# Optimization experiments

Measured on AMD Instinct MI355X. Metric: run time of the kernel, lower is better.

The kernel has to match this reference:

```python
import jax, jax.numpy as jnp
import numpy as np

NEG_INF = -1e9  # masked_fill value from the torch module


def setup_inputs() -> dict:
    key = jax.random.key(0)
    ks = jax.random.split(key, 6)
    n_edges, hidden = 100000, 256
    n_paths, max_len = 20000, 16
    edge_emb = jax.random.normal(ks[0], (n_edges, hidden), dtype=jnp.float32)
    paths = jax.random.randint(ks[1], (n_paths, max_len), 0, n_edges)
    path_lens = jax.random.randint(ks[2], (n_paths,), 0, max_len)  # +1 in reference -> 1..max_len
    path_mask = jax.random.randint(ks[3], (n_paths,), 0, 2)
    # nn.Linear(hidden, 1) parameters
    W = jax.random.normal(ks[4], (1, hidden), dtype=jnp.float32) / np.sqrt(hidden)
    b = jax.random.normal(ks[5], (1,), dtype=jnp.float32) * 0.01
    return {"edge_emb": edge_emb, "paths": paths, "path_lens": path_lens,
            "path_mask": path_mask, "W": W, "b": b, "deterministic": 1}


def reference(edge_emb, paths, path_lens, path_mask, W, b, deterministic):
    # ragged per-path mean: emulate `for p in paths: edge_emb[p].mean(0)` with padded gather
    lens = path_lens + 1                                   # [P], 1..max_len
    pos = jnp.arange(paths.shape[1])                        # [L]
    valid = pos[None, :] < lens[:, None]                    # [P, L]
    gathered = edge_emb[paths]                              # [P, L, H]
    z = jnp.sum(jnp.where(valid[..., None], gathered, 0.0), axis=1) / lens[:, None].astype(edge_emb.dtype)  # [P, H]
    logits = z @ W[0] + b[0]                                # [P]  (Linear(H,1).squeeze())
    logits = jnp.where(path_mask == 0, NEG_INF, logits)
    logp = jax.nn.log_softmax(logits)
    if deterministic:
        p = jnp.argmax(logits)
    else:
        p = jax.random.categorical(jax.random.key(42), logits)
    logprob = logp[p]
    return (p, logprob, z[p])
```

## Files before the change

kernel.cpp:

```cpp
#include <hip/hip_runtime.h>
#include <math.h>
#include <limits.h>

#define NEG_INF -1e9f

__global__ __launch_bounds__(256) void k_edge_dot(
    const float* __restrict__ emb, const float* __restrict__ W,
    float* __restrict__ s, int* __restrict__ counter, int n_edges)
{
    if (blockIdx.x == 0 && threadIdx.x == 0) *counter = 0;
    int wave = (blockIdx.x * (int)blockDim.x + (int)threadIdx.x) >> 6;
    int lane = threadIdx.x & 63;
    if (wave >= n_edges) return;
    const float4 e = ((const float4*)emb)[wave * 64 + lane];
    const float4 w = ((const float4*)W)[lane];
    float d = e.x * w.x + e.y * w.y + e.z * w.z + e.w * w.w;
#pragma unroll
    for (int off = 32; off; off >>= 1) d += __shfl_down(d, off, 64);
    if (lane == 0) s[wave] = d;
}

__global__ __launch_bounds__(256) void k_fused(
    const float* __restrict__ s, const int* __restrict__ paths,
    const int* __restrict__ path_lens, const int* __restrict__ path_mask,
    const float* __restrict__ b, const float* __restrict__ emb,
    float* __restrict__ pmax, int* __restrict__ pidx, float* __restrict__ psum,
    int* __restrict__ counter, float* __restrict__ out,
    int n_paths, int max_len)
{
    __shared__ float rv[4];
    __shared__ int   ri[4];
    __shared__ float rs[4];
    __shared__ float s_bm, s_M, s_S;
    __shared__ int   s_bi, s_P, s_last;

    const int tid = threadIdx.x, lane = tid & 63, wv = tid >> 6;
    const int p = blockIdx.x * 256 + tid;

    float v = -INFINITY; int vi = INT_MAX;
    if (p < n_paths) {
        vi = p;
        if (path_mask[p] == 0) {
            v = NEG_INF;
        } else {
            int len = path_lens[p] + 1;
            float acc = 0.f;
            if (max_len == 16) {
                const int4* pp4 = (const int4*)(paths + (size_t)p * 16);
                int4 a0 = pp4[0], a1 = pp4[1], a2 = pp4[2], a3 = pp4[3];
                int idx[16] = { a0.x, a0.y, a0.z, a0.w, a1.x, a1.y, a1.z, a1.w,
                                a2.x, a2.y, a2.z, a2.w, a3.x, a3.y, a3.z, a3.w };
#pragma unroll
                for (int j = 0; j < 16; ++j) {
                    float t = s[idx[j]];
                    acc += (j < len) ? t : 0.f;
                }
            } else {
                const int* pp = paths + (size_t)p * max_len;
                for (int j = 0; j < len; ++j) acc += s[pp[j]];
            }
            v = acc / (float)len + b[0];
        }
    }

    float bv = v; int bi = vi;
#pragma unroll
    for (int off = 32; off; off >>= 1) {
        float ov = __shfl_down(bv, off, 64);
        int   oi = __shfl_down(bi, off, 64);
        if (ov > bv || (ov == bv && oi < bi)) { bv = ov; bi = oi; }
    }
    if (lane == 0) { rv[wv] = bv; ri[wv] = bi; }
    __syncthreads();
    if (tid == 0) {
        float mv = rv[0]; int mi = ri[0];
        for (int w = 1; w < 4; ++w)
            if (rv[w] > mv || (rv[w] == mv && ri[w] < mi)) { mv = rv[w]; mi = ri[w]; }
        s_bm = mv; s_bi = mi;
    }
    __syncthreads();
    const float bm = s_bm;

    float se = expf(v - bm);
#pragma unroll
    for (int off = 32; off; off >>= 1) se += __shfl_down(se, off, 64);
    if (lane == 0) rs[wv] = se;
    __syncthreads();

    if (tid == 0) {
        pmax[blockIdx.x] = bm;
        pidx[blockIdx.x] = s_bi;
        psum[blockIdx.x] = rs[0] + rs[1] + rs[2] + rs[3];
        __threadfence();
        int tk = atomicAdd(counter, 1);
        s_last = (tk == (int)gridDim.x - 1) ? 1 : 0;
    }
    __syncthreads();
    if (!s_last) return;
    __threadfence();

    const int nb = gridDim.x;
    float mv = -INFINITY; int mi = INT_MAX;
    for (int i = tid; i < nb; i += 256) {
        float t = pmax[i]; int ti = pidx[i];
        if (t > mv || (t == mv && ti < mi)) { mv = t; mi = ti; }
    }
#pragma unroll
    for (int off = 32; off; off >>= 1) {
        float ov = __shfl_down(mv, off, 64);
        int   oi = __shfl_down(mi, off, 64);
        if (ov > mv || (ov == mv && oi < mi)) { mv = ov; mi = oi; }
    }
    if (lane == 0) { rv[wv] = mv; ri[wv] = mi; }
    __syncthreads();
    if (tid == 0) {
        float M = rv[0]; int P = ri[0];
        for (int w = 1; w < 4; ++w)
            if (rv[w] > M || (rv[w] == M && ri[w] < P)) { M = rv[w]; P = ri[w]; }
        s_M = M; s_P = P;
    }
    __syncthreads();
    const float M = s_M; const int P = s_P;

    float sp = 0.f;
    for (int i = tid; i < nb; i += 256)
        sp += psum[i] * expf(pmax[i] - M);
#pragma unroll
    for (int off = 32; off; off >>= 1) sp += __shfl_down(sp, off, 64);
    if (lane == 0) rs[wv] = sp;
    __syncthreads();
    if (tid == 0) s_S = rs[0] + rs[1] + rs[2] + rs[3];
    __syncthreads();

    const int lenP = path_lens[P] + 1;
    const int* pp = paths + (size_t)P * max_len;
    float acc = 0.f;
    for (int j = 0; j < lenP; ++j)
        acc += emb[(size_t)pp[j] * 256 + tid];
    out[2 + tid] = acc / (float)lenP;
    if (tid == 0) { out[0] = (float)P; out[1] = -logf(s_S); }
}

extern "C" void kernel_launch(void* const* d_in, const int* in_sizes, int n_in,
                              void* d_out, int out_size, void* d_ws, size_t ws_size,
                              hipStream_t stream) {
    const float* emb       = (const float*)d_in[0];
    const int*   paths     = (const int*)  d_in[1];
    const int*   path_lens = (const int*)  d_in[2];
    const int*   path_mask = (const int*)  d_in[3];
    const float* W         = (const float*)d_in[4];
    const float* b         = (const float*)d_in[5];

    int hidden  = in_sizes[4];
    int n_edges = in_sizes[0] / hidden;
    int n_paths = in_sizes[2];
    int max_len = in_sizes[1] / n_paths;

    int blocks2 = (n_paths + 255) / 256;

    float* s       = (float*)d_ws;
    float* pmax    = s + n_edges;
    float* psum    = pmax + blocks2;
    int*   pidx    = (int*)(psum + blocks2);
    int*   counter = pidx + blocks2;

    int blocks1 = (n_edges * 64 + 255) / 256;
    k_edge_dot<<<blocks1, 256, 0, stream>>>(emb, W, s, counter, n_edges);

    k_fused<<<blocks2, 256, 0, stream>>>(s, paths, path_lens, path_mask, b, emb,
                                         pmax, pidx, psum, counter,
                                         (float*)d_out, n_paths, max_len);
}
```

Before: 166.0 us.

## Fuse edge dot into path kernel with one wave per path gathering full rows

Removes the separate per-edge dot-product pass over the whole embedding table. Each wave now handles one path: it gathers the full embedding rows with float4 loads, averages them, and dots the mean with W in registers. The grid grows from about 80 blocks of 256 paths to thousands of 4-path blocks, which should hide the latency of the random gathers, and a tiny init kernel resets the counter. In exchange, every valid path reads whole 1KB rows instead of single scalars, and the final block must reduce many more partial results.

```diff
diff --git a/kernel.cpp b/kernel.cpp
--- a/kernel.cpp
+++ b/kernel.cpp
@@ -4,47 +4,31 @@
 
 #define NEG_INF -1e9f
 
-__global__ __launch_bounds__(256) void k_edge_dot(
-    const float* __restrict__ emb, const float* __restrict__ W,
-    float* __restrict__ s, int* __restrict__ counter, int n_edges)
-{
-    if (blockIdx.x == 0 && threadIdx.x == 0) *counter = 0;
-    int wave = (blockIdx.x * (int)blockDim.x + (int)threadIdx.x) >> 6;
-    int lane = threadIdx.x & 63;
-    if (wave >= n_edges) return;
-    const float4 e = ((const float4*)emb)[wave * 64 + lane];
-    const float4 w = ((const float4*)W)[lane];
-    float d = e.x * w.x + e.y * w.y + e.z * w.z + e.w * w.w;
-#pragma unroll
-    for (int off = 32; off; off >>= 1) d += __shfl_down(d, off, 64);
-    if (lane == 0) s[wave] = d;
-}
+__global__ void k_init(int* __restrict__ counter) { *counter = 0; }
 
-__global__ __launch_bounds__(256) void k_fused(
-    const float* __restrict__ s, const int* __restrict__ paths,
+__global__ __launch_bounds__(256) void k_all(
+    const float* __restrict__ emb, const int* __restrict__ paths,
     const int* __restrict__ path_lens, const int* __restrict__ path_mask,
-    const float* __restrict__ b, const float* __restrict__ emb,
+    const float* __restrict__ W, const float* __restrict__ b,
     float* __restrict__ pmax, int* __restrict__ pidx, float* __restrict__ psum,
     int* __restrict__ counter, float* __restrict__ out,
     int n_paths, int max_len)
 {
-    __shared__ float rv[4];
-    __shared__ int   ri[4];
-    __shared__ float rs[4];
-    __shared__ float s_bm, s_M, s_S;
-    __shared__ int   s_bi, s_P, s_last;
+    __shared__ float wvv[4];  __shared__ int wvi[4];  __shared__ int wva[4];
+    __shared__ float rv[4];   __shared__ int ri[4];   __shared__ float rs[4];
+    __shared__ float s_M, s_S;
+    __shared__ int   s_P, s_last;
 
     const int tid = threadIdx.x, lane = tid & 63, wv = tid >> 6;
-    const int p = blockIdx.x * 256 + tid;
+    const int p = blockIdx.x * 4 + wv;
 
-    float v = -INFINITY; int vi = INT_MAX;
+    float v = NEG_INF; int vi = INT_MAX; int act = 0;
     if (p < n_paths) {
-        vi = p;
-        if (path_mask[p] == 0) {
-            v = NEG_INF;
-        } else {
-            int len = path_lens[p] + 1;
-            float acc = 0.f;
+        vi = p; act = 1;
+        if (path_mask[p] != 0) {
+            const int len = path_lens[p] + 1;
+            const float4* emb4 = (const float4*)emb;
+            float4 acc = make_float4(0.f, 0.f, 0.f, 0.f);
             if (max_len == 16) {
                 const int4* pp4 = (const int4*)(paths + (size_t)p * 16);
                 int4 a0 = pp4[0], a1 = pp4[1], a2 = pp4[2], a3 = pp4[3];
@@ -52,45 +36,45 @@
                                 a2.x, a2.y, a2.z, a2.w, a3.x, a3.y, a3.z, a3.w };
 #pragma unroll
                 for (int j = 0; j < 16; ++j) {
-                    float t = s[idx[j]];
-                    acc += (j < len) ? t : 0.f;
+                    int e = (j < len) ? idx[j] : idx[0];
+                    float4 t = emb4[(size_t)e * 64 + lane];
+                    acc.x += (j < len) ? t.x : 0.f;
+                    acc.y += (j < len) ? t.y : 0.f;
+                    acc.z += (j < len) ? t.z : 0.f;
+                    acc.w += (j < len) ? t.w : 0.f;
                 }
             } else {
                 const int* pp = paths + (size_t)p * max_len;
-                for (int j = 0; j < len; ++j) acc += s[pp[j]];
+                for (int j = 0; j < len; ++j) {
+                    float4 t = emb4[(size_t)pp[j] * 64 + lane];
+                    acc.x += t.x; acc.y += t.y; acc.z += t.z; acc.w += t.w;
+                }
             }
-            v = acc / (float)len + b[0];
+            const float fl = (float)len;
+            const float4 w4 = ((const float4*)W)[lane];
+            float d = (acc.x / fl) * w4.x + (acc.y / fl) * w4.y
+                    + (acc.z / fl) * w4.z + (acc.w / fl) * w4.w;
+#pragma unroll
+            for (int off = 32; off; off >>= 1) d += __shfl_down(d, off, 64);
+            v = d + b[0];
         }
     }
-
-    float bv = v; int bi = vi;
-#pragma unroll
-    for (int off = 32; off; off >>= 1) {
-        float ov = __shfl_down(bv, off, 64);
-        int   oi = __shfl_down(bi, off, 64);
-        if (ov > bv || (ov == bv && oi < bi)) { bv = ov; bi = oi; }
-    }
-    if (lane == 0) { rv[wv] = bv; ri[wv] = bi; }
-    __syncthreads();
-    if (tid == 0) {
-        float mv = rv[0]; int mi = ri[0];
-        for (int w = 1; w < 4; ++w)
-            if (rv[w] > mv || (rv[w] == mv && ri[w] < mi)) { mv = rv[w]; mi = ri[w]; }
-        s_bm = mv; s_bi = mi;
-    }
-    __syncthreads();
-    const float bm = s_bm;
-
-    float se = expf(v - bm);
-#pragma unroll
-    for (int off = 32; off; off >>= 1) se += __shfl_down(se, off, 64);
-    if (lane == 0) rs[wv] = se;
+    if (lane == 0) { wvv[wv] = v; wvi[wv] = vi; wva[wv] = act; }
     __syncthreads();
 
     if (tid == 0) {
+        float bm = -INFINITY; int bi = INT_MAX;
+        for (int w = 0; w < 4; ++w)
+            if (wva[w] && (wvv[w] > bm || (wvv[w] == bm && wvi[w] < bi)))
+                { bm = wvv[w]; bi = wvi[w]; }
+        float bs = 0.f;
+        if (bi != INT_MAX) {
+            for (int w = 0; w < 4; ++w)
+                if (wva[w]) bs += expf(wvv[w] - bm);
+        } else { bm = -INFINITY; }
         pmax[blockIdx.x] = bm;
-        pidx[blockIdx.x] = s_bi;
-        psum[blockIdx.x] = rs[0] + rs[1] + rs[2] + rs[3];
+        pidx[blockIdx.x] = bi;
+        psum[blockIdx.x] = bs;
         __threadfence();
         int tk = atomicAdd(counter, 1);
         s_last = (tk == (int)gridDim.x - 1) ? 1 : 0;
@@ -152,22 +136,19 @@
     const float* b         = (const float*)d_in[5];
 
     int hidden  = in_sizes[4];
-    int n_edges = in_sizes[0] / hidden;
     int n_paths = in_sizes[2];
     int max_len = in_sizes[1] / n_paths;
+    (void)hidden;
 
-    int blocks2 = (n_paths + 255) / 256;
+    int blocks = (n_paths + 3) / 4;
 
-    float* s       = (float*)d_ws;
-    float* pmax    = s + n_edges;
-    float* psum    = pmax + blocks2;
-    int*   pidx    = (int*)(psum + blocks2);
-    int*   counter = pidx + blocks2;
+    float* pmax    = (float*)d_ws;
+    float* psum    = pmax + blocks;
+    int*   pidx    = (int*)(psum + blocks);
+    int*   counter = pidx + blocks;
 
-    int blocks1 = (n_edges * 64 + 255) / 256;
-    k_edge_dot<<<blocks1, 256, 0, stream>>>(emb, W, s, counter, n_edges);
-
-    k_fused<<<blocks2, 256, 0, stream>>>(s, paths, path_lens, path_mask, b, emb,
-                                         pmax, pidx, psum, counter,
-                                         (float*)d_out, n_paths, max_len);
+    k_init<<<1, 1, 0, stream>>>(counter);
+    k_all<<<blocks, 256, 0, stream>>>(emb, paths, path_lens, path_mask, W, b,
+                                      pmax, pidx, psum, counter,
+                                      (float*)d_out, n_paths, max_len);
 }
```

New measurement: 368.6 us. +122.0%, slower.

## Compute edge dot products only for edges referenced by unmasked paths

Applied to the files above, without the earlier changes.

Adds a scatter pass that marks edges used by active, in-length path slots, then a grid-stride dot kernel that skips unmarked edges. This avoids reading embedding rows that cannot affect the result. The path-scoring kernel now uses 16 threads per path with 1024-thread blocks and shuffle reductions. The trade-off is an extra memset and an extra kernel launch, plus a divergent flag check per edge.

```diff
diff --git a/kernel.cpp b/kernel.cpp
--- a/kernel.cpp
+++ b/kernel.cpp
@@ -4,23 +4,39 @@
 
 #define NEG_INF -1e9f
 
-__global__ __launch_bounds__(256) void k_edge_dot(
+
+__global__ __launch_bounds__(256) void k_scatter16(
+    const int* __restrict__ paths, const int* __restrict__ path_lens,
+    const int* __restrict__ path_mask, unsigned char* __restrict__ flags,
+    int n_paths)
+{
+    int t = blockIdx.x * 256 + (int)threadIdx.x;
+    if (t >= n_paths * 16) return;
+    int p = t >> 4;
+    if (path_mask[p] == 0) return;
+    if ((t & 15) > path_lens[p]) return;
+    flags[paths[t]] = 1;
+}
+
+__global__ __launch_bounds__(256) void k_dot_flag(
     const float* __restrict__ emb, const float* __restrict__ W,
-    float* __restrict__ s, int* __restrict__ counter, int n_edges)
-{
-    if (blockIdx.x == 0 && threadIdx.x == 0) *counter = 0;
-    int wave = (blockIdx.x * (int)blockDim.x + (int)threadIdx.x) >> 6;
+    const unsigned char* __restrict__ flags, float* __restrict__ s,
+    int n_edges, int n_waves)
+{
+    int wave = (blockIdx.x * 256 + (int)threadIdx.x) >> 6;
     int lane = threadIdx.x & 63;
-    if (wave >= n_edges) return;
-    const float4 e = ((const float4*)emb)[wave * 64 + lane];
-    const float4 w = ((const float4*)W)[lane];
-    float d = e.x * w.x + e.y * w.y + e.z * w.z + e.w * w.w;
-#pragma unroll
-    for (int off = 32; off; off >>= 1) d += __shfl_down(d, off, 64);
-    if (lane == 0) s[wave] = d;
-}
-
-__global__ __launch_bounds__(256) void k_fused(
+    const float4 w4 = ((const float4*)W)[lane];
+    for (int e = wave; e < n_edges; e += n_waves) {
+        if (!flags[e]) continue;
+        float4 r = ((const float4*)emb)[(size_t)e * 64 + lane];
+        float d = r.x * w4.x + r.y * w4.y + r.z * w4.z + r.w * w4.w;
+#pragma unroll
+        for (int off = 32; off; off >>= 1) d += __shfl_down(d, off, 64);
+        if (lane == 0) s[e] = d;
+    }
+}
+
+__global__ __launch_bounds__(1024) void k_fused16(
     const float* __restrict__ s, const int* __restrict__ paths,
     const int* __restrict__ path_lens, const int* __restrict__ path_mask,
     const float* __restrict__ b, const float* __restrict__ emb,
@@ -28,11 +44,131 @@
     int* __restrict__ counter, float* __restrict__ out,
     int n_paths, int max_len)
 {
-    __shared__ float rv[4];
-    __shared__ int   ri[4];
-    __shared__ float rs[4];
-    __shared__ float s_bm, s_M, s_S;
-    __shared__ int   s_bi, s_P, s_last;
+    __shared__ float l_log[64];
+    __shared__ int   l_idx[64];
+    __shared__ float rv[16]; __shared__ int ri[16]; __shared__ float rs[16];
+    __shared__ float s_M, s_S; __shared__ int s_P, s_last;
+
+    const int tid = threadIdx.x, lane = tid & 63, wv = tid >> 6;
+    const int t = blockIdx.x * 1024 + tid;
+    const int p = t >> 4, slot = t & 15;
+
+    float val = 0.f; int mask = 0, len = 1; const int inb = (p < n_paths);
+    if (inb) {
+        mask = path_mask[p];
+        len  = path_lens[p] + 1;
+        if (mask && slot < len) val = s[paths[t]];
+    }
+#pragma unroll
+    for (int m = 1; m <= 8; m <<= 1) val += __shfl_xor(val, m, 16);
+    if (slot == 0) {
+        l_log[tid >> 4] = inb ? (mask ? val / (float)len + b[0] : NEG_INF)
+                              : -INFINITY;
+        l_idx[tid >> 4] = inb ? p : INT_MAX;
+    }
+    __syncthreads();
+
+    if (wv == 0) {
+        float v = l_log[lane]; int vi = l_idx[lane];
+        float bv = v; int bi = vi;
+#pragma unroll
+        for (int off = 32; off; off >>= 1) {
+            float ov = __shfl_down(bv, off, 64);
+            int   oi = __shfl_down(bi, off, 64);
+            if (ov > bv || (ov == bv && oi < bi)) { bv = ov; bi = oi; }
+        }
+        float bm = __shfl(bv, 0, 64);
+        float se = expf(v - bm);
+#pragma unroll
+        for (int off = 32; off; off >>= 1) se += __shfl_down(se, off, 64);
+        if (lane == 0) {
+            pmax[blockIdx.x] = bv;
+            pidx[blockIdx.x] = bi;
+            psum[blockIdx.x] = (bi == INT_MAX) ? 0.f : se;
+            __threadfence();
+            int tk = atomicAdd(counter, 1);
+            s_last = (tk == (int)gridDim.x - 1) ? 1 : 0;
+        }
+    }
+    __syncthreads();
+    if (!s_last) return;
+    __threadfence();
+
+    const int nb = gridDim.x;
+    float mv = -INFINITY; int mi = INT_MAX;
+    for (int i = tid; i < nb; i += 1024) {
+        float tv = pmax[i]; int ti = pidx[i];
+        if (tv > mv || (tv == mv && ti < mi)) { mv = tv; mi = ti; }
+    }
+#pragma unroll
+    for (int off = 32; off; off >>= 1) {
+        float ov = __shfl_down(mv, off, 64);
+        int   oi = __shfl_down(mi, off, 64);
+        if (ov > mv || (ov == mv && oi < mi)) { mv = ov; mi = oi; }
+    }
+    if (lane == 0) { rv[wv] = mv; ri[wv] = mi; }
+    __syncthreads();
+    if (tid == 0) {
+        float M = rv[0]; int P = ri[0];
+        for (int w = 1; w < 16; ++w)
+            if (rv[w] > M || (rv[w] == M && ri[w] < P)) { M = rv[w]; P = ri[w]; }
+        s_M = M; s_P = P;
+    }
+    __syncthreads();
+    const float M = s_M; const int P = s_P;
+
+    float sp = 0.f;
+    for (int i = tid; i < nb; i += 1024)
+        sp += psum[i] * expf(pmax[i] - M);
+#pragma unroll
+    for (int off = 32; off; off >>= 1) sp += __shfl_down(sp, off, 64);
+    if (lane == 0) rs[wv] = sp;
+    __syncthreads();
+    if (tid == 0) {
+        float tot = 0.f;
+        for (int w = 0; w < 16; ++w) tot += rs[w];
+        s_S = tot;
+    }
+    __syncthreads();
+
+    const int lenP = path_lens[P] + 1;
+    const int* pp = paths + (size_t)P * max_len;
+    if (tid < 256) {
+        float acc = 0.f;
+        for (int j = 0; j < lenP; ++j)
+            acc += emb[(size_t)pp[j] * 256 + tid];
+        out[2 + tid] = acc / (float)lenP;
+    }
+    if (tid == 0) { out[0] = (float)P; out[1] = -logf(s_S); }
+}
+
+
+__global__ __launch_bounds__(256) void k_edge_dot(
+    const float* __restrict__ emb, const float* __restrict__ W,
+    float* __restrict__ s, int* __restrict__ counter, int n_edges)
+{
+    if (blockIdx.x == 0 && threadIdx.x == 0) *counter = 0;
+    int wave = (blockIdx.x * (int)blockDim.x + (int)threadIdx.x) >> 6;
+    int lane = threadIdx.x & 63;
+    if (wave >= n_edges) return;
+    const float4 e = ((const float4*)emb)[(size_t)wave * 64 + lane];
+    const float4 w = ((const float4*)W)[lane];
+    float d = e.x * w.x + e.y * w.y + e.z * w.z + e.w * w.w;
+#pragma unroll
+    for (int off = 32; off; off >>= 1) d += __shfl_down(d, off, 64);
+    if (lane == 0) s[wave] = d;
+}
+
+__global__ __launch_bounds__(256) void k_fused_gen(
+    const float* __restrict__ s, const int* __restrict__ paths,
+    const int* __restrict__ path_lens, const int* __restrict__ path_mask,
+    const float* __restrict__ b, const float* __restrict__ emb,
+    float* __restrict__ pmax, int* __restrict__ pidx, float* __restrict__ psum,
+    int* __restrict__ counter, float* __restrict__ out,
+    int n_paths, int max_len)
+{
+    __shared__ float rv[4]; __shared__ int ri[4]; __shared__ float rs[4];
+    __shared__ float s_M, s_S; __shared__ int s_P, s_last;
 
     const int tid = threadIdx.x, lane = tid & 63, wv = tid >> 6;
     const int p = blockIdx.x * 256 + tid;
@@ -40,29 +176,15 @@
     float v = -INFINITY; int vi = INT_MAX;
     if (p < n_paths) {
         vi = p;
-        if (path_mask[p] == 0) {
-            v = NEG_INF;
-        } else {
+        if (path_mask[p] == 0) v = NEG_INF;
+        else {
             int len = path_lens[p] + 1;
+            const int* pp = paths + (size_t)p * max_len;
             float acc = 0.f;
-            if (max_len == 16) {
-                const int4* pp4 = (const int4*)(paths + (size_t)p * 16);
-                int4 a0 = pp4[0], a1 = pp4[1], a2 = pp4[2], a3 = pp4[3];
-                int idx[16] = { a0.x, a0.y, a0.z, a0.w, a1.x, a1.y, a1.z, a1.w,
-                                a2.x, a2.y, a2.z, a2.w, a3.x, a3.y, a3.z, a3.w };
-#pragma unroll
-                for (int j = 0; j < 16; ++j) {
-                    float t = s[idx[j]];
-                    acc += (j < len) ? t : 0.f;
-                }
-            } else {
-                const int* pp = paths + (size_t)p * max_len;
-                for (int j = 0; j < len; ++j) acc += s[pp[j]];
-            }
+            for (int j = 0; j < len; ++j) acc += s[pp[j]];
             v = acc / (float)len + b[0];
         }
     }
-
     float bv = v; int bi = vi;
 #pragma unroll
     for (int off = 32; off; off >>= 1) {
@@ -73,23 +195,21 @@
     if (lane == 0) { rv[wv] = bv; ri[wv] = bi; }
     __syncthreads();
     if (tid == 0) {
-        float mv = rv[0]; int mi = ri[0];
+        float mvv = rv[0]; int mii = ri[0];
         for (int w = 1; w < 4; ++w)
-            if (rv[w] > mv || (rv[w] == mv && ri[w] < mi)) { mv = rv[w]; mi = ri[w]; }
-        s_bm = mv; s_bi = mi;
-    }
-    __syncthreads();
-    const float bm = s_bm;
-
+            if (rv[w] > mvv || (rv[w] == mvv && ri[w] < mii)) { mvv = rv[w]; mii = ri[w]; }
+        s_M = mvv; s_P = mii;
+    }
+    __syncthreads();
+    const float bm = s_M;
     float se = expf(v - bm);
 #pragma unroll
     for (int off = 32; off; off >>= 1) se += __shfl_down(se, off, 64);
     if (lane == 0) rs[wv] = se;
     __syncthreads();
-
     if (tid == 0) {
         pmax[blockIdx.x] = bm;
-        pidx[blockIdx.x] = s_bi;
+        pidx[blockIdx.x] = s_P;
         psum[blockIdx.x] = rs[0] + rs[1] + rs[2] + rs[3];
         __threadfence();
         int tk = atomicAdd(counter, 1);
@@ -102,8 +222,8 @@
     const int nb = gridDim.x;
     float mv = -INFINITY; int mi = INT_MAX;
     for (int i = tid; i < nb; i += 256) {
-        float t = pmax[i]; int ti = pidx[i];
-        if (t > mv || (t == mv && ti < mi)) { mv = t; mi = ti; }
+        float tv = pmax[i]; int ti = pidx[i];
+        if (tv > mv || (tv == mv && ti < mi)) { mv = tv; mi = ti; }
     }
 #pragma unroll
     for (int off = 32; off; off >>= 1) {
@@ -121,7 +241,6 @@
     }
     __syncthreads();
     const float M = s_M; const int P = s_P;
-
     float sp = 0.f;
     for (int i = tid; i < nb; i += 256)
         sp += psum[i] * expf(pmax[i] - M);
@@ -134,12 +253,15 @@
 
     const int lenP = path_lens[P] + 1;
     const int* pp = paths + (size_t)P * max_len;
-    float acc = 0.f;
-    for (int j = 0; j < lenP; ++j)
-        acc += emb[(size_t)pp[j] * 256 + tid];
-    out[2 + tid] = acc / (float)lenP;
+    if (tid < 256) {
+        float acc = 0.f;
+        for (int j = 0; j < lenP; ++j)
+            acc += emb[(size_t)pp[j] * 256 + tid];
+        out[2 + tid] = acc / (float)lenP;
+    }
     if (tid == 0) { out[0] = (float)P; out[1] = -logf(s_S); }
 }
+
 
 extern "C" void kernel_launch(void* const* d_in, const int* in_sizes, int n_in,
                               void* d_out, int out_size, void* d_ws, size_t ws_size,
@@ -156,18 +278,41 @@
     int n_paths = in_sizes[2];
     int max_len = in_sizes[1] / n_paths;
 
-    int blocks2 = (n_paths + 255) / 256;
-
-    float* s       = (float*)d_ws;
-    float* pmax    = s + n_edges;
-    float* psum    = pmax + blocks2;
-    int*   pidx    = (int*)(psum + blocks2);
-    int*   counter = pidx + blocks2;
-
-    int blocks1 = (n_edges * 64 + 255) / 256;
-    k_edge_dot<<<blocks1, 256, 0, stream>>>(emb, W, s, counter, n_edges);
-
-    k_fused<<<blocks2, 256, 0, stream>>>(s, paths, path_lens, path_mask, b, emb,
-                                         pmax, pidx, psum, counter,
-                                         (float*)d_out, n_paths, max_len);
-}
+    if (max_len == 16 && hidden == 256) {
+        size_t flags_pad = ((size_t)n_edges + 255) & ~(size_t)255;
+        unsigned char* flags = (unsigned char*)d_ws;
+        int*   counter = (int*)(flags + flags_pad);
+        float* s       = (float*)(flags + flags_pad + 256);
+        int nb3 = (n_paths * 16 + 1023) / 1024;
+        float* pmax = s + n_edges;
+        float* psum = pmax + nb3;
+        int*   pidx = (int*)(psum + nb3);
+
+        hipMemsetAsync(d_ws, 0, flags_pad + sizeof(int), stream);
+
+        int blocksS = (n_paths * 16 + 255) / 256;
+        k_scatter16<<<blocksS, 256, 0, stream>>>(paths, path_lens, path_mask,
+                                                 flags, n_paths);
+
+        int blocksD = 4096;
+        k_dot_flag<<<blocksD, 256, 0, stream>>>(emb, W, flags, s,
+                                                n_edges, blocksD * 4);
+
+        k_fused16<<<nb3, 1024, 0, stream>>>(s, paths, path_lens, path_mask,
+                                            b, emb, pmax, pidx, psum, counter,
+                                            (float*)d_out, n_paths, max_len);
+    } else {
+        float* s = (float*)d_ws;
+        int blocks2 = (n_paths + 255) / 256;
+        float* pmax    = s + n_edges;
+        float* psum    = pmax + blocks2;
+        int*   pidx    = (int*)(psum + blocks2);
+        int*   counter = pidx + blocks2;
+
+        int blocks1 = (n_edges * 64 + 255) / 256;
+        k_edge_dot<<<blocks1, 256, 0, stream>>>(emb, W, s, counter, n_edges);
+        k_fused_gen<<<blocks2, 256, 0, stream>>>(s, paths, path_lens, path_mask,
+                                                 b, emb, pmax, pidx, psum, counter,
+                                                 (float*)d_out, n_paths, max_len);
+    }
+}
```

New measurement: 176.1 us. 6.1% more time.
